# Optimization experiments

Measured on AMD Instinct MI355X. Metric: run time of the kernel, lower is better.

The kernel has to match this reference:

```python
import jax, jax.numpy as jnp
import numpy as np
from jax import lax

SD = 16  # sample_duration
POOL_KS = (SD, SD * 3 // 4, SD // 2, SD // 4)  # (16, 12, 8, 4)


def conv3d_same(x, w, b):
    # x: [B,C,T,H,W], w: [O,I,3,3,3]
    y = lax.conv_general_dilated(
        x, w, window_strides=(1, 1, 1), padding=[(1, 1), (1, 1), (1, 1)],
        dimension_numbers=("NCDHW", "OIDHW", "NCDHW"))
    return y + b[None, :, None, None, None]


def maxpool_t(x, k):
    # MaxPool3d((k,1,1), stride=1): max over sliding temporal window
    return lax.reduce_window(x, -jnp.inf, lax.max,
                             (1, 1, k, 1, 1), (1, 1, 1, 1, 1), "VALID")


def head1x1(x, w, b):
    # 1x1x1 Conv3d as einsum; x: [B,C,T,H,W], w: [O,C]
    return jnp.einsum("bcthw,oc->bothw", x, w) + b[None, :, None, None, None]


def cls_prob(score):
    # _RPN.reshape(x,2) -> softmax(dim=1) -> reshape back to [B,30,T,H,W]
    B, C, T, H, W = score.shape
    s2 = score.reshape(B, 2, (C * T) // 2, H, W)
    p = jax.nn.softmax(s2, axis=1)
    return p.reshape(B, C, T, H, W)


def setup_inputs() -> dict:
    key = jax.random.key(0)
    ks = jax.random.split(key, 12)
    din, B, H, W = 512, 2, 28, 28
    s = 0.05
    return {
        "base_feat": jax.random.normal(ks[0], (B, din, SD, H, W), jnp.float32),
        "im_info": jnp.ones((B, 3), jnp.float32) * 448.0,
        "gt_boxes": jax.random.uniform(ks[1], (B, 20, 5), jnp.float32),
        "gt_rois": jax.random.uniform(ks[2], (B, 20, SD, 5), jnp.float32),
        "W_conv": jax.random.normal(ks[3], (din, din, 3, 3, 3), jnp.float32) * 0.01,
        "b_conv": jnp.zeros((din,), jnp.float32),
        "W_cls": jax.random.normal(ks[4], (30, din), jnp.float32) * s,
        "b_cls": jnp.zeros((30,), jnp.float32),
        "W_bbox": jax.random.normal(ks[5], (960, din), jnp.float32) * s,
        "b_bbox": jnp.zeros((960,), jnp.float32),
        "W_bbox_34": jax.random.normal(ks[6], (720, din), jnp.float32) * s,
        "b_bbox_34": jnp.zeros((720,), jnp.float32),
        "W_bbox_2": jax.random.normal(ks[7], (480, din), jnp.float32) * s,
        "b_bbox_2": jnp.zeros((480,), jnp.float32),
        "W_bbox_4": jax.random.normal(ks[8], (240, din), jnp.float32) * s,
        "b_bbox_4": jnp.zeros((240,), jnp.float32),
    }


def reference(base_feat, im_info, gt_boxes, gt_rois,
              W_conv, b_conv, W_cls, b_cls,
              W_bbox, b_bbox, W_bbox_34, b_bbox_34,
              W_bbox_2, b_bbox_2, W_bbox_4, b_bbox_4):
    # RPN conv + relu
    x = jax.nn.relu(conv3d_same(base_feat, W_conv, b_conv))
    # four temporal max-pool branches (T' = 1, 5, 9, 13)
    pools = [maxpool_t(x, k) for k in POOL_KS]
    # NOTE: original code applies the SAME RPN_cls_score conv to all branches
    probs = tuple(cls_prob(head1x1(p, W_cls, b_cls)) for p in pools)
    bbox_ws = [(W_bbox, b_bbox), (W_bbox_34, b_bbox_34),
               (W_bbox_2, b_bbox_2), (W_bbox_4, b_bbox_4)]
    bboxes = tuple(head1x1(p, w, b) for p, (w, b) in zip(pools, bbox_ws))
    return probs + bboxes
```

## Files before the change

### kernel.cpp

```cpp
#include <hip/hip_runtime.h>

typedef unsigned short u16;
typedef unsigned int   u32;
typedef __bf16  bf16x8 __attribute__((ext_vector_type(8)));
typedef float   f32x4  __attribute__((ext_vector_type(4)));

__device__ __forceinline__ float bf2f(u16 u) {
    u32 v = ((u32)u) << 16;
    return __builtin_bit_cast(float, v);
}
__device__ __forceinline__ u16 f2bf(float f) {
    u32 u = __builtin_bit_cast(u32, f);
    return (u16)((u + 0x7FFFu + ((u >> 16) & 1u)) >> 16);
}
__device__ __forceinline__ float ldf(const void* p, long i, int f32) {
    return f32 ? ((const float*)p)[i] : bf2f(((const u16*)p)[i]);
}
__device__ __forceinline__ int is_f32(const u32* im) {
    return im[0] == 0x43E00000u;
}
__device__ __forceinline__ void gl2lds16(const u16* g, u16* l) {
    __builtin_amdgcn_global_load_lds(
        (const __attribute__((address_space(1))) void*)g,
        (__attribute__((address_space(3))) void*)l, 16, 0, 0);
}

__global__ void zero_halo(u16* __restrict__ xpad)
{
    int i = blockIdx.x * 256 + threadIdx.x;
    if (i < 230400) {
        int c8 = i & 63; int pos = i >> 6;
        int p = pos % 900; pos /= 900;
        int t = (pos & 1) * 17; int b = pos >> 1;
        long o = (((long)(b * 18 + t) * 900) + p) * 512 + c8 * 8;
        *(uint4*)&xpad[o] = uint4{0u, 0u, 0u, 0u};
        return;
    }
    i -= 230400;
    if (i < 122880) {
        int c8 = i & 63; int pos = i >> 6;
        int w = pos % 30; pos /= 30;
        int h = (pos & 1) * 29; pos >>= 1;
        int t = pos % 16 + 1; int b = pos / 16;
        long o = ((((long)(b * 18 + t) * 30 + h) * 30) + w) * 512 + c8 * 8;
        *(uint4*)&xpad[o] = uint4{0u, 0u, 0u, 0u};
        return;
    }
    i -= 122880;
    if (i < 114688) {
        int c8 = i & 63; int pos = i >> 6;
        int w = (pos & 1) * 29; pos >>= 1;
        int h = pos % 28 + 1; pos /= 28;
        int t = pos % 16 + 1; int b = pos / 16;
        long o = ((((long)(b * 18 + t) * 30 + h) * 30) + w) * 512 + c8 * 8;
        *(uint4*)&xpad[o] = uint4{0u, 0u, 0u, 0u};
    }
}

__global__ void pad_fill(const void* __restrict__ src, u16* __restrict__ xpad,
                         const u32* __restrict__ im)
{
    const int f32 = is_f32(im);
    __shared__ u16 lds[56 * 40];
    int blk = blockIdx.x;
    const int h2  = blk % 14;  blk /= 14;
    const int c32 = blk & 15;  blk >>= 4;
    const int t   = blk & 15;
    const int b   = blk >> 4;
    const int tid = threadIdx.x;
    const long sbase = ((long)(b * 512 + c32 * 32) * 16 + t) * 784 + h2 * 56;
    #pragma unroll
    for (int it = tid; it < 1792; it += 256) {
        const int c = it / 56, p = it - c * 56;
        float v = f32 ? ((const float*)src)[sbase + (long)c * 12544 + p]
                      : bf2f(((const u16*)src)[sbase + (long)c * 12544 + p]);
        lds[p * 40 + c] = f2bf(v);
    }
    __syncthreads();
    if (tid < 224) {
        const int p = tid >> 2, g = tid & 3;
        const int h = h2 * 2 + p / 28, w = p % 28;
        const long o = (((long)(b * 18 + t + 1) * 30 + h + 1) * 30 + (w + 1)) * 512
                       + c32 * 32 + g * 8;
        *(uint4*)&xpad[o] = *(const uint4*)&lds[p * 40 + g * 8];
    }
}

__global__ void wt_transform(const void* __restrict__ wconv, u16* __restrict__ wt,
                             const u32* __restrict__ im)
{
    const int f32 = is_f32(im);
    __shared__ u16 lds[256 * 28];
    const int tid = threadIdx.x;
    const int pair_base = blockIdx.x * 256;
    const long s0 = (long)pair_base * 27;
    for (int it = tid; it < 256 * 27; it += 256) {
        const int p = it / 27, o = it - p * 27;
        float v = f32 ? ((const float*)wconv)[s0 + it]
                      : bf2f(((const u16*)wconv)[s0 + it]);
        lds[p * 28 + o] = f2bf(v);
    }
    __syncthreads();
    #pragma unroll
    for (int off = 0; off < 27; ++off)
        wt[(long)off * 262144 + pair_base + tid] = lds[tid * 28 + off];
}

__global__ void cvt_all(const void* s0, const void* s1, const void* s2,
                        const void* s3, const void* s4,
                        const void* b0, const void* b1, const void* b2,
                        const void* b3, const void* b4, const void* b5,
                        u16* __restrict__ whd, float* __restrict__ bfs,
                        const u32* __restrict__ im)
{
    const int f32 = is_f32(im);
    int i = blockIdx.x * 256 + threadIdx.x;
    if (i < 1244160) {
        const void* s; long j;
        if      (i < 15360)   { s = s0; j = i; }
        else if (i < 506880)  { s = s1; j = i - 15360; }
        else if (i < 875520)  { s = s2; j = i - 506880; }
        else if (i < 1121280) { s = s3; j = i - 875520; }
        else                  { s = s4; j = i - 1121280; }
        whd[i] = f2bf(ldf(s, j, f32));
        return;
    }
    i -= 1244160;
    if (i >= 2942) return;
    float v;
    if      (i < 512)  v = ldf(b0, i, f32);
    else if (i < 542)  v = ldf(b1, i - 512, f32);
    else if (i < 1502) v = ldf(b2, i - 542, f32);
    else if (i < 2222) v = ldf(b3, i - 1502, f32);
    else if (i < 2702) v = ldf(b4, i - 2222, f32);
    else               v = ldf(b5, i - 2702, f32);
    bfs[i] = v;
}

__global__ __launch_bounds__(512, 2) void conv_gemm256(
    const u16* __restrict__ xpad, const u16* __restrict__ wt,
    const float* __restrict__ bfs, u16* __restrict__ y)
{
    __shared__ u16 smem[65536];
    const int tid = threadIdx.x;

    const int bx  = blockIdx.x;
    const int xcd = bx & 7, pos = bx >> 3;
    const int L   = (xcd < 4 ? xcd * 25 : 100 + (xcd - 4) * 24) + pos;
    const int m_base = (L & 1) * 256;
    const int n_base = (L >> 1) * 256;

    const int rq8 = tid >> 3;
    const int sw  = (((tid & 7) ^ (rq8 & 7))) * 8;
    const u16* pa = wt + (long)(m_base + rq8) * 512 + sw;

    long sbj[4];
    #pragma unroll
    for (int j = 0; j < 4; ++j) {
        const int n = n_base + j * 64 + rq8;
        int b = n / 12544, r = n % 12544;
        int t = r / 784,   q = r % 784;
        int h = q / 28,    w = q % 28;
        const int sa = ((b * 18 + t) * 30 + h) * 30 + w;
        sbj[j] = (long)sa * 512 + sw;
    }

    const int lane = tid & 63, wid = tid >> 6;
    const int l16 = lane & 15, quad = lane >> 4;
    const int wm = wid >> 2;
    const int wn = wid & 3;
    const int x7 = l16 & 7;
    const int o0 = (quad ^ x7) * 8;
    const int o1 = ((4 + quad) ^ x7) * 8;
    int rowA[8], rowB[4];
    #pragma unroll
    for (int mi = 0; mi < 8; ++mi) rowA[mi] = (wm * 128 + mi * 16 + l16) * 64;
    #pragma unroll
    for (int ni = 0; ni < 4; ++ni) rowB[ni] = 16384 + (wn * 64 + ni * 16 + l16) * 64;

    f32x4 acc[8][4] = {};

    {
        u16* dst = smem;
        #pragma unroll
        for (int j = 0; j < 4; ++j)
            gl2lds16(pa + (long)j * 32768, dst + j * 4096 + tid * 8);
        #pragma unroll
        for (int j = 0; j < 4; ++j)
            gl2lds16(xpad + sbj[j], dst + 16384 + j * 4096 + tid * 8);
    }

    for (int kt = 0; kt < 216; ++kt) {
        asm volatile("s_waitcnt vmcnt(0)" ::: "memory");
        asm volatile("s_barrier" ::: "memory");
        const u16* buf = smem + (kt & 1) * 32768;

        bf16x8 af[8], bfr[4];
        #pragma unroll
        for (int mi = 0; mi < 4; ++mi)
            af[mi] = *(const bf16x8*)&buf[rowA[mi] + o0];
        #pragma unroll
        for (int ni = 0; ni < 4; ++ni)
            bfr[ni] = *(const bf16x8*)&buf[rowB[ni] + o0];
        #pragma unroll
        for (int mi = 4; mi < 8; ++mi)
            af[mi] = *(const bf16x8*)&buf[rowA[mi] + o0];

        if (kt < 215) {
            const int kts = kt + 1;
            const int tap = kts >> 3, kc = kts & 7;
            const int kd = tap / 9, r9 = tap - kd * 9;
            const int kh = r9 / 3,  kw = r9 - kh * 3;
            const long aoff = (long)tap * 262144 + kc * 64;
            const long boff = (long)(kd * 900 + kh * 30 + kw) * 512 + kc * 64;
            u16* dst = smem + ((kts & 1) << 15);
            #pragma unroll
            for (int j = 0; j < 4; ++j)
                gl2lds16(pa + aoff + (long)j * 32768, dst + j * 4096 + tid * 8);
            #pragma unroll
            for (int j = 0; j < 4; ++j)
                gl2lds16(xpad + sbj[j] + boff, dst + 16384 + j * 4096 + tid * 8);
        }

        __builtin_amdgcn_s_setprio(1);
        #pragma unroll
        for (int mi = 0; mi < 8; ++mi)
            #pragma unroll
            for (int ni = 0; ni < 4; ++ni)
                acc[mi][ni] = __builtin_amdgcn_mfma_f32_16x16x32_bf16(
                    af[mi], bfr[ni], acc[mi][ni], 0, 0, 0);
        __builtin_amdgcn_s_setprio(0);

        bf16x8 ag[8], bgr[4];
        #pragma unroll
        for (int mi = 0; mi < 8; ++mi)
            ag[mi] = *(const bf16x8*)&buf[rowA[mi] + o1];
        #pragma unroll
        for (int ni = 0; ni < 4; ++ni)
            bgr[ni] = *(const bf16x8*)&buf[rowB[ni] + o1];

        __builtin_amdgcn_s_setprio(1);
        #pragma unroll
        for (int mi = 0; mi < 8; ++mi)
            #pragma unroll
            for (int ni = 0; ni < 4; ++ni)
                acc[mi][ni] = __builtin_amdgcn_mfma_f32_16x16x32_bf16(
                    ag[mi], bgr[ni], acc[mi][ni], 0, 0, 0);
        __builtin_amdgcn_s_setprio(0);
    }

    #pragma unroll
    for (int mi = 0; mi < 8; ++mi) {
        const int mrow = m_base + wm * 128 + mi * 16 + quad * 4;
        float bias[4];
        #pragma unroll
        for (int r = 0; r < 4; ++r) bias[r] = bfs[mrow + r];
        #pragma unroll
        for (int ni = 0; ni < 4; ++ni) {
            const int ng = n_base + wn * 64 + ni * 16 + l16;
            f32x4 a = acc[mi][ni];
            u16 o0v = f2bf(fmaxf(a[0] + bias[0], 0.f));
            u16 o1v = f2bf(fmaxf(a[1] + bias[1], 0.f));
            u16 o2v = f2bf(fmaxf(a[2] + bias[2], 0.f));
            u16 o3v = f2bf(fmaxf(a[3] + bias[3], 0.f));
            uint2 pv;
            pv.x = (u32)o0v | ((u32)o1v << 16);
            pv.y = (u32)o2v | ((u32)o3v << 16);
            *(uint2*)&y[(long)ng * 512 + mrow] = pv;
        }
    }
}

__device__ __forceinline__ uint2 max4(uint2 A, uint2 Bv)
{
    const u16* a = (const u16*)&A;
    const u16* b = (const u16*)&Bv;
    uint2 R;
    u16* r = (u16*)&R;
    #pragma unroll
    for (int i = 0; i < 4; ++i) r[i] = (bf2f(a[i]) >= bf2f(b[i])) ? a[i] : b[i];
    return R;
}

__global__ void pool_all(const u16* __restrict__ y, u16* __restrict__ p4,
                         u16* __restrict__ p8, u16* __restrict__ p12,
                         u16* __restrict__ p16)
{
    int g = blockIdx.x * 256 + threadIdx.x;
    if (g >= 200704) return;
    const int c4 = g & 127;
    int pos = g >> 7;
    const int hw = pos % 784; const int b = pos / 784;
    const u16* src = y + ((long)(b * 16) * 784 + hw) * 512 + c4 * 4;
    uint2 v[16];
    #pragma unroll
    for (int t = 0; t < 16; ++t)
        v[t] = *(const uint2*)(src + (long)t * 401408);
    uint2 pr[15];
    #pragma unroll
    for (int t = 0; t < 15; ++t) pr[t] = max4(v[t], v[t + 1]);
    uint2 qd[13];
    #pragma unroll
    for (int t = 0; t < 13; ++t) qd[t] = max4(pr[t], pr[t + 2]);
    uint2 e8[9];
    #pragma unroll
    for (int t = 0; t < 9; ++t) e8[t] = max4(qd[t], qd[t + 4]);
    uint2 e12[5];
    #pragma unroll
    for (int t = 0; t < 5; ++t) e12[t] = max4(e8[t], qd[t + 8]);
    uint2 e16 = max4(e8[0], e8[8]);

    const long col = (long)hw * 512 + c4 * 4;
    #pragma unroll
    for (int t = 0; t < 13; ++t)
        *(uint2*)&p4[((long)(b * 13 + t) * 784) * 512 + col] = qd[t];
    #pragma unroll
    for (int t = 0; t < 9; ++t)
        *(uint2*)&p8[((long)(b * 9 + t) * 784) * 512 + col] = e8[t];
    #pragma unroll
    for (int t = 0; t < 5; ++t)
        *(uint2*)&p12[((long)(b * 5 + t) * 784) * 512 + col] = e12[t];
    *(uint2*)&p16[((long)b * 784) * 512 + col] = e16;
}

__global__ __launch_bounds__(256, 2) void heads_gemm(
    const u16* __restrict__ p16, const u16* __restrict__ p12,
    const u16* __restrict__ p8,  const u16* __restrict__ p4,
    const u16* __restrict__ wcls, const u16* __restrict__ wb1,
    const u16* __restrict__ wb34, const u16* __restrict__ wb2,
    const u16* __restrict__ wb4,  const float* __restrict__ bfs,
    float* __restrict__ clsr, void* __restrict__ outv,
    const u32* __restrict__ im)
{
    const int f32 = is_f32(im);
    int bid = blockIdx.x;
    const u16* pool; const u16* wbp; int Ti, CH, nt, mt; long boff, coff, ooff;
    if (bid < 104)      {             nt = bid % 13;  mt = bid / 13;  pool = p16; wbp = wb1;  Ti = 1;  CH = 960; boff = 542;  coff = 0;      ooff = 1317120; }
    else if (bid < 476) { bid -= 104; nt = bid % 62;  mt = bid / 62;  pool = p12; wbp = wb34; Ti = 5;  CH = 720; boff = 1502; coff = 47040;  ooff = 2822400; }
    else if (bid < 920) { bid -= 476; nt = bid % 111; mt = bid / 111; pool = p8;  wbp = wb2;  Ti = 9;  CH = 480; boff = 2222; coff = 282240; ooff = 8467200; }
    else                { bid -= 920; nt = bid % 160; mt = bid / 160; pool = p4;  wbp = wb4;  Ti = 13; CH = 240; boff = 2702; coff = 705600; ooff = 15240960; }
    const int M = 30 + CH;
    const int THW = Ti * 784;
    const int N = 2 * THW;
    const int n_base = nt * 128;
    const int m_base = mt * 128;

    __shared__ u16 lds[16384];
    const int tid = threadIdx.x;
    const int lane = tid & 63;
    const int wid  = tid >> 6;
    const int quad = lane >> 4;
    const int l16  = lane & 15;
    const int wm = (wid & 1) * 64;
    const int wn = (wid >> 1) * 64;

    const int srow = tid >> 2;
    const int kk   = (((tid & 3) ^ ((tid >> 3) & 3))) * 8;

    const u16* arow[2]; const u16* brow[2];
    #pragma unroll
    for (int i = 0; i < 2; ++i) {
        int m = m_base + i * 64 + srow; if (m > M - 1) m = M - 1;
        arow[i] = ((m < 30) ? (wcls + m * 512) : (wbp + (m - 30) * 512)) + kk;
        int n = n_base + i * 64 + srow; if (n > N - 1) n = N - 1;
        brow[i] = pool + (long)n * 512 + kk;
    }

    const int co = (quad ^ ((l16 >> 1) & 3)) * 8;
    int rowA[4], rowB[4];
    #pragma unroll
    for (int i = 0; i < 4; ++i) {
        rowA[i] = (wm + i * 16 + l16) * 32 + co;
        rowB[i] = 4096 + (wn + i * 16 + l16) * 32 + co;
    }

    #pragma unroll
    for (int i = 0; i < 2; ++i)
        gl2lds16(arow[i], &lds[i * 2048 + tid * 8]);
    #pragma unroll
    for (int i = 0; i < 2; ++i)
        gl2lds16(brow[i], &lds[4096 + i * 2048 + tid * 8]);

    f32x4 acc[4][4] = {};
    for (int kc = 0; kc < 16; ++kc) {
        asm volatile("s_waitcnt vmcnt(0)" ::: "memory");
        asm volatile("s_barrier" ::: "memory");
        const u16* buf = lds + (kc & 1) * 8192;
        bf16x8 af[4], bfr[4];
        #pragma unroll
        for (int mi = 0; mi < 4; ++mi)
            af[mi]  = *(const bf16x8*)&buf[rowA[mi]];
        #pragma unroll
        for (int ni = 0; ni < 4; ++ni)
            bfr[ni] = *(const bf16x8*)&buf[rowB[ni]];
        if (kc < 15) {
            const int kcol = (kc + 1) * 32;
            u16* dst = lds + ((kc + 1) & 1) * 8192 + tid * 8;
            #pragma unroll
            for (int i = 0; i < 2; ++i)
                gl2lds16(arow[i] + kcol, dst + i * 2048);
            #pragma unroll
            for (int i = 0; i < 2; ++i)
                gl2lds16(brow[i] + kcol, dst + 4096 + i * 2048);
        }
        __builtin_amdgcn_s_setprio(1);
        #pragma unroll
        for (int mi = 0; mi < 4; ++mi)
            #pragma unroll
            for (int ni = 0; ni < 4; ++ni)
                acc[mi][ni] = __builtin_amdgcn_mfma_f32_16x16x32_bf16(
                    af[mi], bfr[ni], acc[mi][ni], 0, 0, 0);
        __builtin_amdgcn_s_setprio(0);
    }

    const float* bcls = bfs + 512;
    const float* bb   = bfs + boff;
    #pragma unroll
    for (int mi = 0; mi < 4; ++mi) {
        const int mrow = m_base + wm + mi * 16 + quad * 4;
        #pragma unroll
        for (int ni = 0; ni < 4; ++ni) {
            const int ng = n_base + wn + ni * 16 + l16;
            if (ng >= N) continue;
            const int b  = ng / THW;
            const int rr = ng % THW;
            f32x4 a = acc[mi][ni];
            #pragma unroll
            for (int r = 0; r < 4; ++r) {
                const int m = mrow + r;
                if (m >= M) break;
                const float bias = (m < 30) ? bcls[m] : bb[m - 30];
                const float v = a[r] + bias;
                if (m < 30) {
                    clsr[coff + ((long)(b * 30 + m)) * THW + rr] = v;
                } else {
                    const long oi = ooff + ((long)(b * CH + (m - 30))) * THW + rr;
                    if (f32) ((float*)outv)[oi] = v;
                    else     ((u16*)outv)[oi]   = f2bf(v);
                }
            }
        }
    }
}

__global__ void softmax_all(const float* __restrict__ clsr,
                            void* __restrict__ outv, const u32* __restrict__ im)
{
    const int f32 = is_f32(im);
    int g = blockIdx.x * 256 + threadIdx.x;
    if (g >= 658560) return;
    int Ti; long off;
    if      (g < 23520)  { Ti = 1;  off = 0; }
    else if (g < 141120) { Ti = 5;  off = 47040;  g -= 23520; }
    else if (g < 352800) { Ti = 9;  off = 282240; g -= 141120; }
    else                 { Ti = 13; off = 705600; g -= 352800; }
    const int THW = Ti * 784;
    const int rr = g % THW;
    int r2 = g / THW;
    const int j = r2 % 15; const int b = r2 / 15;
    const long i0 = off + ((long)(b * 30 + j)) * THW + rr;
    const long i1 = off + ((long)(b * 30 + j + 15)) * THW + rr;
    const float s0 = clsr[i0], s1 = clsr[i1];
    const float mx = fmaxf(s0, s1);
    const float e0 = __expf(s0 - mx), e1 = __expf(s1 - mx);
    const float inv = 1.0f / (e0 + e1);
    if (f32) {
        ((float*)outv)[i0] = e0 * inv;
        ((float*)outv)[i1] = e1 * inv;
    } else {
        ((u16*)outv)[i0] = f2bf(e0 * inv);
        ((u16*)outv)[i1] = f2bf(e1 * inv);
    }
}

extern "C" void kernel_launch(void* const* d_in, const int* in_sizes, int n_in,
                              void* d_out, int out_size, void* d_ws, size_t ws_size,
                              hipStream_t stream)
{
    const void* base_feat = d_in[0];
    const u32*  im_info   = (const u32*)d_in[1];
    const void* W_conv    = d_in[4];
    const void* b_conv    = d_in[5];
    const void* W_cls     = d_in[6];
    const void* b_cls     = d_in[7];
    const void* W_bbox    = d_in[8];
    const void* b_bbox    = d_in[9];
    const void* W_bbox34  = d_in[10];
    const void* b_bbox34  = d_in[11];
    const void* W_bbox2   = d_in[12];
    const void* b_bbox2   = d_in[13];
    const void* W_bbox4   = d_in[14];
    const void* b_bbox4   = d_in[15];

    char* ws = (char*)d_ws;
    u16*   xpad = (u16*)  (ws + 0);
    u16*   wt   = (u16*)  (ws + 33177600);
    u16*   y    = (u16*)  (ws + 47333376);
    u16*   p4   = (u16*)  (ws + 73023488);
    u16*   p8   = (u16*)  (ws + 93896704);
    u16*   p12  = (u16*)  (ws + 108347392);
    u16*   p16  = (u16*)  (ws + 116375552);
    float* clsr = (float*)(ws + 117981184);
    u16*   whd  = (u16*)  (ws + 123249728);
    float* bfs  = (float*)(ws + 125738048);

    u16* w_cls_b  = whd;
    u16* w_b1_b   = whd + 15360;
    u16* w_b34_b  = whd + 506880;
    u16* w_b2_b   = whd + 875520;
    u16* w_b4_b   = whd + 1121280;

    zero_halo<<<1828, 256, 0, stream>>>(xpad);
    pad_fill<<<7168, 256, 0, stream>>>(base_feat, xpad, im_info);
    wt_transform<<<1024, 256, 0, stream>>>(W_conv, wt, im_info);
    cvt_all<<<4873, 256, 0, stream>>>(W_cls, W_bbox, W_bbox34, W_bbox2, W_bbox4,
                                      b_conv, b_cls, b_bbox, b_bbox34, b_bbox2,
                                      b_bbox4, whd, bfs, im_info);

    conv_gemm256<<<196, 512, 0, stream>>>(xpad, wt, bfs, y);

    pool_all<<<784, 256, 0, stream>>>(y, p4, p8, p12, p16);

    heads_gemm<<<1400, 256, 0, stream>>>(p16, p12, p8, p4,
                                         w_cls_b, w_b1_b, w_b34_b, w_b2_b, w_b4_b,
                                         bfs, clsr, d_out, im_info);

    softmax_all<<<2573, 256, 0, stream>>>(clsr, d_out, im_info);
}
```

Measured before the change: 569.4 us.

## Fuse softmax into heads GEMM, triple-buffer its K loop, merge pad kernels

The class-score softmax now runs in the heads GEMM epilogue: the 30 cls rows are staged in LDS and normalised in place, so the float scratch buffer and the separate softmax launch go away. The heads GEMM K loop moves from double to triple buffering, keeping two tiles in flight and waiting with vmcnt(4) instead of draining all loads. The zero_halo and pad_fill kernels are merged into one launch. The GEMM uses more LDS per block, which may lower occupancy.

Measured after the change: 562.3 us. No clear change (-1.2%).

```diff
diff --git a/kernel.cpp b/kernel.cpp
--- a/kernel.cpp
+++ b/kernel.cpp
@@ -25,43 +25,42 @@
         (__attribute__((address_space(3))) void*)l, 16, 0, 0);
 }
 
-__global__ void zero_halo(u16* __restrict__ xpad)
-{
-    int i = blockIdx.x * 256 + threadIdx.x;
-    if (i < 230400) {
-        int c8 = i & 63; int pos = i >> 6;
-        int p = pos % 900; pos /= 900;
-        int t = (pos & 1) * 17; int b = pos >> 1;
-        long o = (((long)(b * 18 + t) * 900) + p) * 512 + c8 * 8;
-        *(uint4*)&xpad[o] = uint4{0u, 0u, 0u, 0u};
+__global__ void pad_zero_fill(const void* __restrict__ src, u16* __restrict__ xpad,
+                              const u32* __restrict__ im)
+{
+    __shared__ u16 lds[56 * 40];
+    if (blockIdx.x >= 7168) {
+        int i = (blockIdx.x - 7168) * 256 + threadIdx.x;
+        if (i < 230400) {
+            int c8 = i & 63; int pos = i >> 6;
+            int p = pos % 900; pos /= 900;
+            int t = (pos & 1) * 17; int b = pos >> 1;
+            long o = (((long)(b * 18 + t) * 900) + p) * 512 + c8 * 8;
+            *(uint4*)&xpad[o] = uint4{0u, 0u, 0u, 0u};
+            return;
+        }
+        i -= 230400;
+        if (i < 122880) {
+            int c8 = i & 63; int pos = i >> 6;
+            int w = pos % 30; pos /= 30;
+            int h = (pos & 1) * 29; pos >>= 1;
+            int t = pos % 16 + 1; int b = pos / 16;
+            long o = ((((long)(b * 18 + t) * 30 + h) * 30) + w) * 512 + c8 * 8;
+            *(uint4*)&xpad[o] = uint4{0u, 0u, 0u, 0u};
+            return;
+        }
+        i -= 122880;
+        if (i < 114688) {
+            int c8 = i & 63; int pos = i >> 6;
+            int w = (pos & 1) * 29; pos >>= 1;
+            int h = pos % 28 + 1; pos /= 28;
+            int t = pos % 16 + 1; int b = pos / 16;
+            long o = ((((long)(b * 18 + t) * 30 + h) * 30) + w) * 512 + c8 * 8;
+            *(uint4*)&xpad[o] = uint4{0u, 0u, 0u, 0u};
+        }
         return;
     }
-    i -= 230400;
-    if (i < 122880) {
-        int c8 = i & 63; int pos = i >> 6;
-        int w = pos % 30; pos /= 30;
-        int h = (pos & 1) * 29; pos >>= 1;
-        int t = pos % 16 + 1; int b = pos / 16;
-        long o = ((((long)(b * 18 + t) * 30 + h) * 30) + w) * 512 + c8 * 8;
-        *(uint4*)&xpad[o] = uint4{0u, 0u, 0u, 0u};
-        return;
-    }
-    i -= 122880;
-    if (i < 114688) {
-        int c8 = i & 63; int pos = i >> 6;
-        int w = (pos & 1) * 29; pos >>= 1;
-        int h = pos % 28 + 1; pos /= 28;
-        int t = pos % 16 + 1; int b = pos / 16;
-        long o = ((((long)(b * 18 + t) * 30 + h) * 30) + w) * 512 + c8 * 8;
-        *(uint4*)&xpad[o] = uint4{0u, 0u, 0u, 0u};
-    }
-}
-
-__global__ void pad_fill(const void* __restrict__ src, u16* __restrict__ xpad,
-                         const u32* __restrict__ im)
-{
     const int f32 = is_f32(im);
-    __shared__ u16 lds[56 * 40];
     int blk = blockIdx.x;
     const int h2  = blk % 14;  blk /= 14;
     const int c32 = blk & 15;  blk >>= 4;
@@ -329,8 +328,7 @@
     const u16* __restrict__ wcls, const u16* __restrict__ wb1,
     const u16* __restrict__ wb34, const u16* __restrict__ wb2,
     const u16* __restrict__ wb4,  const float* __restrict__ bfs,
-    float* __restrict__ clsr, void* __restrict__ outv,
-    const u32* __restrict__ im)
+    void* __restrict__ outv, const u32* __restrict__ im)
 {
     const int f32 = is_f32(im);
     int bid = blockIdx.x;
@@ -345,7 +343,7 @@
     const int n_base = nt * 128;
     const int m_base = mt * 128;
 
-    __shared__ u16 lds[16384];
+    __shared__ u16 lds[24576];
     const int tid = threadIdx.x;
     const int lane = tid & 63;
     const int wid  = tid >> 6;
@@ -380,12 +378,19 @@
     #pragma unroll
     for (int i = 0; i < 2; ++i)
         gl2lds16(brow[i], &lds[4096 + i * 2048 + tid * 8]);
+    #pragma unroll
+    for (int i = 0; i < 2; ++i)
+        gl2lds16(arow[i] + 32, &lds[8192 + i * 2048 + tid * 8]);
+    #pragma unroll
+    for (int i = 0; i < 2; ++i)
+        gl2lds16(brow[i] + 32, &lds[8192 + 4096 + i * 2048 + tid * 8]);
 
     f32x4 acc[4][4] = {};
-    for (int kc = 0; kc < 16; ++kc) {
-        asm volatile("s_waitcnt vmcnt(0)" ::: "memory");
+    int cb = 0;
+    for (int kc = 0; kc < 15; ++kc) {
+        asm volatile("s_waitcnt vmcnt(4)" ::: "memory");
         asm volatile("s_barrier" ::: "memory");
-        const u16* buf = lds + (kc & 1) * 8192;
+        const u16* buf = lds + cb * 8192;
         bf16x8 af[4], bfr[4];
         #pragma unroll
         for (int mi = 0; mi < 4; ++mi)
@@ -393,9 +398,10 @@
         #pragma unroll
         for (int ni = 0; ni < 4; ++ni)
             bfr[ni] = *(const bf16x8*)&buf[rowB[ni]];
-        if (kc < 15) {
-            const int kcol = (kc + 1) * 32;
-            u16* dst = lds + ((kc + 1) & 1) * 8192 + tid * 8;
+        if (kc < 14) {
+            const int kcol = (kc + 2) * 32;
+            int nb = cb + 2; if (nb >= 3) nb -= 3;
+            u16* dst = lds + nb * 8192 + tid * 8;
             #pragma unroll
             for (int i = 0; i < 2; ++i)
                 gl2lds16(arow[i] + kcol, dst + i * 2048);
@@ -411,8 +417,29 @@
                 acc[mi][ni] = __builtin_amdgcn_mfma_f32_16x16x32_bf16(
                     af[mi], bfr[ni], acc[mi][ni], 0, 0, 0);
         __builtin_amdgcn_s_setprio(0);
-    }
-
+        cb = (cb + 1 == 3) ? 0 : cb + 1;
+    }
+    {
+        asm volatile("s_waitcnt vmcnt(0)" ::: "memory");
+        asm volatile("s_barrier" ::: "memory");
+        const u16* buf = lds + cb * 8192;
+        bf16x8 af[4], bfr[4];
+        #pragma unroll
+        for (int mi = 0; mi < 4; ++mi)
+            af[mi]  = *(const bf16x8*)&buf[rowA[mi]];
+        #pragma unroll
+        for (int ni = 0; ni < 4; ++ni)
+            bfr[ni] = *(const bf16x8*)&buf[rowB[ni]];
+        #pragma unroll
+        for (int mi = 0; mi < 4; ++mi)
+            #pragma unroll
+            for (int ni = 0; ni < 4; ++ni)
+                acc[mi][ni] = __builtin_amdgcn_mfma_f32_16x16x32_bf16(
+                    af[mi], bfr[ni], acc[mi][ni], 0, 0, 0);
+    }
+
+    __syncthreads();
+    float* smf = (float*)lds;
     const float* bcls = bfs + 512;
     const float* bb   = bfs + boff;
     #pragma unroll
@@ -429,11 +456,10 @@
             for (int r = 0; r < 4; ++r) {
                 const int m = mrow + r;
                 if (m >= M) break;
-                const float bias = (m < 30) ? bcls[m] : bb[m - 30];
-                const float v = a[r] + bias;
                 if (m < 30) {
-                    clsr[coff + ((long)(b * 30 + m)) * THW + rr] = v;
+                    smf[m * 128 + (wn + ni * 16 + l16)] = a[r] + bcls[m];
                 } else {
+                    const float v = a[r] + bb[m - 30];
                     const long oi = ooff + ((long)(b * CH + (m - 30))) * THW + rr;
                     if (f32) ((float*)outv)[oi] = v;
                     else     ((u16*)outv)[oi]   = f2bf(v);
@@ -441,35 +467,28 @@
             }
         }
     }
-}
-
-__global__ void softmax_all(const float* __restrict__ clsr,
-                            void* __restrict__ outv, const u32* __restrict__ im)
-{
-    const int f32 = is_f32(im);
-    int g = blockIdx.x * 256 + threadIdx.x;
-    if (g >= 658560) return;
-    int Ti; long off;
-    if      (g < 23520)  { Ti = 1;  off = 0; }
-    else if (g < 141120) { Ti = 5;  off = 47040;  g -= 23520; }
-    else if (g < 352800) { Ti = 9;  off = 282240; g -= 141120; }
-    else                 { Ti = 13; off = 705600; g -= 352800; }
-    const int THW = Ti * 784;
-    const int rr = g % THW;
-    int r2 = g / THW;
-    const int j = r2 % 15; const int b = r2 / 15;
-    const long i0 = off + ((long)(b * 30 + j)) * THW + rr;
-    const long i1 = off + ((long)(b * 30 + j + 15)) * THW + rr;
-    const float s0 = clsr[i0], s1 = clsr[i1];
-    const float mx = fmaxf(s0, s1);
-    const float e0 = __expf(s0 - mx), e1 = __expf(s1 - mx);
-    const float inv = 1.0f / (e0 + e1);
-    if (f32) {
-        ((float*)outv)[i0] = e0 * inv;
-        ((float*)outv)[i1] = e1 * inv;
-    } else {
-        ((u16*)outv)[i0] = f2bf(e0 * inv);
-        ((u16*)outv)[i1] = f2bf(e1 * inv);
+    __syncthreads();
+    if (m_base == 0) {
+        for (int p = tid; p < 1920; p += 256) {
+            const int j = p >> 7, col = p & 127;
+            const int ng = n_base + col;
+            if (ng >= N) continue;
+            const float s0 = smf[j * 128 + col];
+            const float s1 = smf[(j + 15) * 128 + col];
+            const float mx = fmaxf(s0, s1);
+            const float e0 = __expf(s0 - mx), e1 = __expf(s1 - mx);
+            const float inv = 1.0f / (e0 + e1);
+            const int b = ng / THW, rr = ng % THW;
+            const long i0 = coff + ((long)(b * 30 + j)) * THW + rr;
+            const long i1 = coff + ((long)(b * 30 + j + 15)) * THW + rr;
+            if (f32) {
+                ((float*)outv)[i0] = e0 * inv;
+                ((float*)outv)[i1] = e1 * inv;
+            } else {
+                ((u16*)outv)[i0] = f2bf(e0 * inv);
+                ((u16*)outv)[i1] = f2bf(e1 * inv);
+            }
+        }
     }
 }
 
@@ -500,7 +519,6 @@
     u16*   p8   = (u16*)  (ws + 93896704);
     u16*   p12  = (u16*)  (ws + 108347392);
     u16*   p16  = (u16*)  (ws + 116375552);
-    float* clsr = (float*)(ws + 117981184);
     u16*   whd  = (u16*)  (ws + 123249728);
     float* bfs  = (float*)(ws + 125738048);
 
@@ -510,8 +528,7 @@
     u16* w_b2_b   = whd + 875520;
     u16* w_b4_b   = whd + 1121280;
 
-    zero_halo<<<1828, 256, 0, stream>>>(xpad);
-    pad_fill<<<7168, 256, 0, stream>>>(base_feat, xpad, im_info);
+    pad_zero_fill<<<8996, 256, 0, stream>>>(base_feat, xpad, im_info);
     wt_transform<<<1024, 256, 0, stream>>>(W_conv, wt, im_info);
     cvt_all<<<4873, 256, 0, stream>>>(W_cls, W_bbox, W_bbox34, W_bbox2, W_bbox4,
                                       b_conv, b_cls, b_bbox, b_bbox34, b_bbox2,
@@ -523,7 +540,5 @@
 
     heads_gemm<<<1400, 256, 0, stream>>>(p16, p12, p8, p4,
                                          w_cls_b, w_b1_b, w_b34_b, w_b2_b, w_b4_b,
-                                         bfs, clsr, d_out, im_info);
-
-    softmax_all<<<2573, 256, 0, stream>>>(clsr, d_out, im_info);
-}
+                                         bfs, d_out, im_info);
+}
```
